# Performance work log

Hardware: AMD Instinct MI355X
Metric: run time of the kernel (lower is better)

Reference implementation:

```python
import jax, jax.numpy as jnp
import numpy as np

N_WIRES = 4
DIM = 1 << N_WIRES  # 16
N_PATCH = 14 * 14   # 196


def _random_unitary_16(seed=0):
    # Deterministic surrogate for tq.RandomLayer(n_ops=8): a fixed random
    # real orthogonal 16x16 operator applied to the 4-qubit state.
    rng = np.random.default_rng(seed)
    q, _ = np.linalg.qr(rng.standard_normal((DIM, DIM)))
    return jnp.asarray(q, dtype=jnp.float32)


def _linear_params(rng, fan_in, fan_out):
    bound = 1.0 / np.sqrt(fan_in)
    w = rng.uniform(-bound, bound, size=(fan_out, fan_in)).astype(np.float32)
    b = rng.uniform(-bound, bound, size=(fan_out,)).astype(np.float32)
    return jnp.asarray(w), jnp.asarray(b)


def setup_inputs() -> dict:
    key = jax.random.key(0)
    x = jax.random.normal(key, (8192, 784), dtype=jnp.float32)
    rng = np.random.default_rng(1)
    fc1_w, fc1_b = _linear_params(rng, 784, 120)
    fc2_w, fc2_b = _linear_params(rng, 120, 84)
    fc3_w, fc3_b = _linear_params(rng, 84, 1)
    return {
        "x": x,
        "U": _random_unitary_16(),
        "fc1_w": fc1_w, "fc1_b": fc1_b,
        "fc2_w": fc2_w, "fc2_b": fc2_b,
        "fc3_w": fc3_w, "fc3_b": fc3_b,
    }


def _quantum_filter(x, U):
    # x: [b, 784] -> 2x2 patches in row-major order, per-patch wire data
    # [x[r,c], x[r,c+1], x[r+1,c], x[r+1,c+1]]
    b = x.shape[0]
    xp = x.reshape(b, 14, 2, 14, 2).transpose(0, 1, 3, 2, 4).reshape(b, N_PATCH, N_WIRES)
    # Encoder: RY(theta_w) on wire w starting from |0000> -> product state
    c = jnp.cos(0.5 * xp)  # [b, p, 4]
    s = jnp.sin(0.5 * xp)
    a = jnp.stack([c, s], axis=-1)  # [b, p, 4, 2] per-wire amplitudes
    psi = jnp.einsum("bpi,bpj,bpk,bpl->bpijkl",
                     a[:, :, 0], a[:, :, 1], a[:, :, 2], a[:, :, 3])
    psi = psi.reshape(b, N_PATCH, DIM)  # wire 0 = most significant bit
    # Fixed random layer (16x16 unitary)
    psi = jnp.einsum("ij,bpj->bpi", U, psi)
    # PauliZ expectation per wire: sum_i |psi_i|^2 * (1 - 2*bit_w(i))
    idx = jnp.arange(DIM)
    bits = (idx[:, None] >> (N_WIRES - 1 - jnp.arange(N_WIRES))) & 1  # [16, 4]
    zsign = (1 - 2 * bits).astype(psi.dtype)
    meas = jnp.einsum("bpi,iw->bpw", psi * psi, zsign)  # [b, p, 4]
    return meas.reshape(b, N_PATCH * N_WIRES)  # [b, 784]


def reference(x, U, fc1_w, fc1_b, fc2_w, fc2_b, fc3_w, fc3_b):
    feats = _quantum_filter(x, U)
    h = jax.nn.relu(feats @ fc1_w.T + fc1_b)
    h = jax.nn.relu(h @ fc2_w.T + fc2_b)
    logits = (h @ fc3_w.T + fc3_b)[:, 0]  # [b], matches inputs.squeeze()
    # = P(|1>) = (1 + sin(theta)) / 2 (analytic, shot-noise-free)
    exp_val = 0.5 * (1.0 + jnp.sin(logits))
    p = jax.nn.sigmoid(exp_val)
    return jnp.concatenate([p, 1.0 - p], axis=-1)  # [2*b], matches torch.cat on 1-D
```

## Files before the change

kernel.cpp:

```cpp
#include <hip/hip_runtime.h>
#include <hip/hip_bf16.h>
#include <math.h>


#define BATCH   8192
#define NPATCH  196
#define ROWS    8
#define NITEMS  (ROWS * NPATCH)
#define KPAD    800
#define FLD     808
#define H1LD    132

typedef __attribute__((ext_vector_type(8))) short bfrag;
typedef __attribute__((ext_vector_type(4))) float f32x4;

static __device__ __forceinline__ unsigned short f2bf(float f) {
    __hip_bfloat16 h = __float2bfloat16(f);
    return __builtin_bit_cast(unsigned short, h);
}
static __device__ __forceinline__ unsigned int pkbf(float lo, float hi) {
    return ((unsigned int)f2bf(hi) << 16) | (unsigned int)f2bf(lo);
}

__global__ __launch_bounds__(256) void w1prep_kernel(
    const float* __restrict__ w1, unsigned short* __restrict__ w1B)
{
    int t = blockIdx.x * 256 + threadIdx.x;
    if (t >= 128 * KPAD) return;
    int n = t / KPAD;
    int k = t - n * KPAD;
    float v = (n < 120 && k < 784) ? w1[n * 784 + k] : 0.f;
    w1B[t] = f2bf(v);
}

__global__ __launch_bounds__(256, 7) void mega_kernel(
    const float* __restrict__ x, const float* __restrict__ U,
    const unsigned short* __restrict__ w1B,
    const float* __restrict__ b1,
    const float* __restrict__ w2, const float* __restrict__ b2,
    const float* __restrict__ w3, const float* __restrict__ b3,
    float* __restrict__ out)
{
    __shared__ __align__(16) unsigned short featsL[ROWS * FLD];
    __shared__ __align__(16) unsigned char pool[8192];

    unsigned short (*psiL)[64][16] =
        reinterpret_cast<unsigned short (*)[64][16]>(pool);
    float* h1L = reinterpret_cast<float*>(pool);
    float* h2L = reinterpret_cast<float*>(pool + ROWS * H1LD * 4);

    const int tid  = threadIdx.x;
    const int lane = tid & 63;
    const int wv   = tid >> 6;
    const int lrow = lane & 15;
    const int lgrp = lane >> 4;
    const int m0   = blockIdx.x * ROWS;

    if (tid < ROWS * 16)
        featsL[(tid >> 4) * FLD + 784 + (tid & 15)] = 0;

    bfrag Uf;
    {
        union { bfrag f; unsigned int u[4]; } uu;
        if (lgrp < 2) {
            float4 a = *reinterpret_cast<const float4*>(U + lrow * 16 + lgrp * 8);
            float4 b = *reinterpret_cast<const float4*>(U + lrow * 16 + lgrp * 8 + 4);
            uu.u[0] = pkbf(a.x, a.y); uu.u[1] = pkbf(a.z, a.w);
            uu.u[2] = pkbf(b.x, b.y); uu.u[3] = pkbf(b.z, b.w);
        } else {
            uu.u[0] = uu.u[1] = uu.u[2] = uu.u[3] = 0u;
        }
        Uf = uu.f;
    }

    for (int c = wv; c < (NITEMS + 63) / 64; c += 4) {
        int item = c * 64 + lane;
        int it   = item < NITEMS - 1 ? item : NITEMS - 1;
        int r  = it / NPATCH;
        int p  = it - r * NPATCH;
        int pr = p / 14;
        int pc = p - pr * 14;
        const float* xr = x + (size_t)(m0 + r) * 784 + pr * 56 + pc * 2;
        float2 xa = *reinterpret_cast<const float2*>(xr);
        float2 xb = *reinterpret_cast<const float2*>(xr + 28);

        float s0 = __sinf(0.5f * xa.x), c0 = __cosf(0.5f * xa.x);
        float s1 = __sinf(0.5f * xa.y), c1 = __cosf(0.5f * xa.y);
        float s2 = __sinf(0.5f * xb.x), c2 = __cosf(0.5f * xb.x);
        float s3 = __sinf(0.5f * xb.y), c3 = __cosf(0.5f * xb.y);

        float t01[4] = {c0 * c1, c0 * s1, s0 * c1, s0 * s1};
        float t23[4] = {c2 * c3, c2 * s3, s2 * c3, s2 * s3};

        unsigned int pw[8];
#pragma unroll
        for (int q = 0; q < 8; ++q) {
            float plo = t01[(2 * q) >> 2]     * t23[(2 * q) & 3];
            float phv = t01[(2 * q + 1) >> 2] * t23[(2 * q + 1) & 3];
            pw[q] = pkbf(plo, phv);
        }
        *reinterpret_cast<uint4*>(&psiL[wv][lane][0]) =
            make_uint4(pw[0], pw[1], pw[2], pw[3]);
        *reinterpret_cast<uint4*>(&psiL[wv][lane][8]) =
            make_uint4(pw[4], pw[5], pw[6], pw[7]);

#pragma unroll
        for (int sub = 0; sub < 4; ++sub) {
            bfrag Bf = {};
            if (lgrp < 2)
                Bf = *reinterpret_cast<const bfrag*>(
                    &psiL[wv][sub * 16 + lrow][lgrp * 8]);
            f32x4 dz = {0.f, 0.f, 0.f, 0.f};
            f32x4 d = __builtin_amdgcn_mfma_f32_16x16x32_bf16(Uf, Bf, dz, 0, 0, 0);
            float q0 = d[0] * d[0], q1 = d[1] * d[1];
            float q2 = d[2] * d[2], q3 = d[3] * d[3];
            float sAll = (q0 + q1) + (q2 + q3);
            float uu2  = (q0 + q1) - (q2 + q3);
            float vv2  = (q0 - q1) + (q2 - q3);
            float t    = __shfl_xor(sAll, 16);
            float Aa   = sAll + t;
            float Bb   = (lane & 16) ? (t - sAll) : (sAll - t);
            t = __shfl_xor(Aa, 32);
            float mw0 = (lane & 32) ? (t - Aa) : (Aa - t);
            float mw1 = Bb + __shfl_xor(Bb, 32);
            float u16 = uu2 + __shfl_xor(uu2, 16);
            float mw2 = u16 + __shfl_xor(u16, 32);
            float v16 = vv2 + __shfl_xor(vv2, 16);
            float mw3 = v16 + __shfl_xor(v16, 32);

            int item16 = c * 64 + sub * 16 + lrow;
            if (lgrp == 0 && item16 < NITEMS) {
                int rr = item16 / NPATCH;
                int pp = item16 - rr * NPATCH;
                ushort4 o;
                o.x = f2bf(mw0); o.y = f2bf(mw1);
                o.z = f2bf(mw2); o.w = f2bf(mw3);
                *reinterpret_cast<ushort4*>(&featsL[rr * FLD + pp * 4]) = o;
            }
        }
    }
    __syncthreads();

    {
        const unsigned short* fA = &featsL[(lrow & 7) * FLD + lgrp * 8];
        const unsigned short* bp0 =
            w1B + (size_t)(wv * 32 + lrow) * KPAD + lgrp * 8;
        const unsigned short* bp1 = bp0 + 16 * KPAD;

        f32x4 acc0 = {}, acc1 = {};
        for (int k0 = 0; k0 < KPAD; k0 += 32) {
            bfrag a   = *reinterpret_cast<const bfrag*>(fA + k0);
            bfrag b0  = *reinterpret_cast<const bfrag*>(bp0 + k0);
            bfrag b1f = *reinterpret_cast<const bfrag*>(bp1 + k0);
            acc0 = __builtin_amdgcn_mfma_f32_16x16x32_bf16(a, b0, acc0, 0, 0, 0);
            acc1 = __builtin_amdgcn_mfma_f32_16x16x32_bf16(a, b1f, acc1, 0, 0, 0);
        }
        f32x4 accs[2] = {acc0, acc1};
#pragma unroll
        for (int nj = 0; nj < 2; ++nj) {
            int col = wv * 32 + nj * 16 + lrow;
            if (col < 120) {
                float bias = b1[col];
#pragma unroll
                for (int rr2 = 0; rr2 < 4; ++rr2) {
                    int row = lgrp * 4 + rr2;
                    if (row < ROWS)
                        h1L[row * H1LD + col] =
                            fmaxf(accs[nj][rr2] + bias, 0.f);
                }
            }
        }
    }
    __syncthreads();

    for (int e = tid; e < ROWS * 21; e += 256) {
        int r  = e / 21;
        int nq = e - r * 21;
        int n0 = nq * 4;
        float4 bias = *reinterpret_cast<const float4*>(b2 + n0);
        float accv[4] = {bias.x, bias.y, bias.z, bias.w};
#pragma unroll
        for (int kq = 0; kq < 30; ++kq) {
            float4 a = *reinterpret_cast<const float4*>(&h1L[r * H1LD + kq * 4]);
#pragma unroll
            for (int nn = 0; nn < 4; ++nn) {
                const float4 wvv = *reinterpret_cast<const float4*>(
                    w2 + (size_t)(n0 + nn) * 120 + kq * 4);
                accv[nn] = fmaf(a.x, wvv.x, accv[nn]);
                accv[nn] = fmaf(a.y, wvv.y, accv[nn]);
                accv[nn] = fmaf(a.z, wvv.z, accv[nn]);
                accv[nn] = fmaf(a.w, wvv.w, accv[nn]);
            }
        }
        float4 o;
        o.x = fmaxf(accv[0], 0.f);
        o.y = fmaxf(accv[1], 0.f);
        o.z = fmaxf(accv[2], 0.f);
        o.w = fmaxf(accv[3], 0.f);
        *reinterpret_cast<float4*>(&h2L[r * 84 + n0]) = o;
    }
    __syncthreads();

    if (tid < ROWS) {
        int r = tid;
        float acc = b3[0];
#pragma unroll
        for (int kq = 0; kq < 21; ++kq) {
            float4 a   = *reinterpret_cast<const float4*>(&h2L[r * 84 + kq * 4]);
            float4 wvv = *reinterpret_cast<const float4*>(w3 + kq * 4);
            acc = fmaf(a.x, wvv.x, acc);
            acc = fmaf(a.y, wvv.y, acc);
            acc = fmaf(a.z, wvv.z, acc);
            acc = fmaf(a.w, wvv.w, acc);
        }
        float ev = 0.5f * (1.0f + __sinf(acc));
        float pp = 1.0f / (1.0f + __expf(-ev));
        out[m0 + r]         = pp;
        out[BATCH + m0 + r] = 1.0f - pp;
    }
}

extern "C" void kernel_launch(void* const* d_in, const int* in_sizes, int n_in,
                              void* d_out, int out_size, void* d_ws, size_t ws_size,
                              hipStream_t stream)
{
    (void)in_sizes; (void)n_in; (void)out_size; (void)ws_size;
    const float* x  = (const float*)d_in[0];
    const float* U  = (const float*)d_in[1];
    const float* w1 = (const float*)d_in[2];
    const float* b1 = (const float*)d_in[3];
    const float* w2 = (const float*)d_in[4];
    const float* b2 = (const float*)d_in[5];
    const float* w3 = (const float*)d_in[6];
    const float* b3 = (const float*)d_in[7];
    float* out = (float*)d_out;

    unsigned short* w1B = (unsigned short*)d_ws;

    w1prep_kernel<<<dim3((128 * KPAD + 255) / 256), dim3(256), 0, stream>>>(w1, w1B);
    mega_kernel<<<dim3(BATCH / ROWS), dim3(256), 0, stream>>>(
        x, U, w1B, b1, w2, b2, w3, b3, out);
}
```

Baseline: 142.5 us.

## Compute PauliZ reduction with a second MFMA instead of lane shuffles

Uses the 16x16x16 bf16 MFMA for the unitary apply, with no zero-padded K half, then squares the amplitudes and runs a second MFMA against a Z-sign matrix to get the four wire expectations. This replaces the shuffle-based butterfly reduction. It also switches to __sincosf and lowers the launch-bounds occupancy hint from 7 to 4 blocks. The squared amplitudes are now rounded to bf16 before the reduction, which adds precision loss. The lower occupancy hint may change register allocation and residency.

```diff
diff --git a/kernel.cpp b/kernel.cpp
--- a/kernel.cpp
+++ b/kernel.cpp
@@ -12,7 +12,14 @@
 #define H1LD    132
 
 typedef __attribute__((ext_vector_type(8))) short bfrag;
+typedef __attribute__((ext_vector_type(4))) short bfrag4;
 typedef __attribute__((ext_vector_type(4))) float f32x4;
+
+#if __has_builtin(__builtin_amdgcn_mfma_f32_16x16x16bf16_1k)
+#define USE_X16 1
+#else
+#define USE_X16 0
+#endif
 
 static __device__ __forceinline__ unsigned short f2bf(float f) {
     __hip_bfloat16 h = __float2bfloat16(f);
@@ -33,7 +40,7 @@
     w1B[t] = f2bf(v);
 }
 
-__global__ __launch_bounds__(256, 7) void mega_kernel(
+__global__ __launch_bounds__(256, 4) void mega_kernel(
     const float* __restrict__ x, const float* __restrict__ U,
     const unsigned short* __restrict__ w1B,
     const float* __restrict__ b1,
@@ -59,6 +66,33 @@
     if (tid < ROWS * 16)
         featsL[(tid >> 4) * FLD + 784 + (tid & 15)] = 0;
 
+#if USE_X16
+    bfrag4 Uf16;
+    {
+        union { bfrag4 f; unsigned int u[2]; } uu;
+        float4 a = *reinterpret_cast<const float4*>(U + lrow * 16 + lgrp * 4);
+        uu.u[0] = pkbf(a.x, a.y);
+        uu.u[1] = pkbf(a.z, a.w);
+        Uf16 = uu.f;
+    }
+    bfrag4 Zf;
+    {
+        union { bfrag4 f; unsigned int u[2]; } zz;
+        if (lrow < 4) {
+            float z[4];
+#pragma unroll
+            for (int j = 0; j < 4; ++j) {
+                int k = 4 * lgrp + j;
+                z[j] = ((k >> (3 - lrow)) & 1) ? -1.f : 1.f;
+            }
+            zz.u[0] = pkbf(z[0], z[1]);
+            zz.u[1] = pkbf(z[2], z[3]);
+        } else {
+            zz.u[0] = zz.u[1] = 0u;
+        }
+        Zf = zz.f;
+    }
+#else
     bfrag Uf;
     {
         union { bfrag f; unsigned int u[4]; } uu;
@@ -72,6 +106,7 @@
         }
         Uf = uu.f;
     }
+#endif
 
     for (int c = wv; c < (NITEMS + 63) / 64; c += 4) {
         int item = c * 64 + lane;
@@ -84,10 +119,11 @@
         float2 xa = *reinterpret_cast<const float2*>(xr);
         float2 xb = *reinterpret_cast<const float2*>(xr + 28);
 
-        float s0 = __sinf(0.5f * xa.x), c0 = __cosf(0.5f * xa.x);
-        float s1 = __sinf(0.5f * xa.y), c1 = __cosf(0.5f * xa.y);
-        float s2 = __sinf(0.5f * xb.x), c2 = __cosf(0.5f * xb.x);
-        float s3 = __sinf(0.5f * xb.y), c3 = __cosf(0.5f * xb.y);
+        float s0, c0, s1, c1, s2, c2, s3, c3;
+        __sincosf(0.5f * xa.x, &s0, &c0);
+        __sincosf(0.5f * xa.y, &s1, &c1);
+        __sincosf(0.5f * xb.x, &s2, &c2);
+        __sincosf(0.5f * xb.y, &s3, &c3);
 
         float t01[4] = {c0 * c1, c0 * s1, s0 * c1, s0 * s1};
         float t23[4] = {c2 * c3, c2 * s3, s2 * c3, s2 * s3};
@@ -106,6 +142,27 @@
 
 #pragma unroll
         for (int sub = 0; sub < 4; ++sub) {
+            int item16 = c * 64 + sub * 16 + lrow;
+#if USE_X16
+            bfrag4 Pf = *reinterpret_cast<const bfrag4*>(
+                &psiL[wv][sub * 16 + lrow][lgrp * 4]);
+            f32x4 dz = {0.f, 0.f, 0.f, 0.f};
+            f32x4 d = __builtin_amdgcn_mfma_f32_16x16x16bf16_1k(
+                Uf16, Pf, dz, 0, 0, 0);
+            union { bfrag4 f; unsigned int u[2]; } qq;
+            qq.u[0] = pkbf(d[0] * d[0], d[1] * d[1]);
+            qq.u[1] = pkbf(d[2] * d[2], d[3] * d[3]);
+            f32x4 m = __builtin_amdgcn_mfma_f32_16x16x16bf16_1k(
+                Zf, qq.f, dz, 0, 0, 0);
+            if (lgrp == 0 && item16 < NITEMS) {
+                int rr = item16 / NPATCH;
+                int pp = item16 - rr * NPATCH;
+                uint2 o2;
+                o2.x = pkbf(m[0], m[1]);
+                o2.y = pkbf(m[2], m[3]);
+                *reinterpret_cast<uint2*>(&featsL[rr * FLD + pp * 4]) = o2;
+            }
+#else
             bfrag Bf = {};
             if (lgrp < 2)
                 Bf = *reinterpret_cast<const bfrag*>(
@@ -127,8 +184,6 @@
             float mw2 = u16 + __shfl_xor(u16, 32);
             float v16 = vv2 + __shfl_xor(vv2, 16);
             float mw3 = v16 + __shfl_xor(v16, 32);
-
-            int item16 = c * 64 + sub * 16 + lrow;
             if (lgrp == 0 && item16 < NITEMS) {
                 int rr = item16 / NPATCH;
                 int pp = item16 - rr * NPATCH;
@@ -137,6 +192,7 @@
                 o.z = f2bf(mw2); o.w = f2bf(mw3);
                 *reinterpret_cast<ushort4*>(&featsL[rr * FLD + pp * 4]) = o;
             }
+#endif
         }
     }
     __syncthreads();
```

Result: faster. 136.0 us (-4.6%).
